# Kernel optimization log

Measured on AMD Instinct MI355X. Metric: run time of the kernel, lower is better.

Reference implementation:

```python
import jax, jax.numpy as jnp
import numpy as np

N_NODES = 50000
N_EDGES = 1600000
IN_C, HID_C, OUT_C = 64, 64, 7


def setup_inputs() -> dict:
    key = jax.random.key(0)
    ks = jax.random.split(key, 8)
    x = jax.random.normal(ks[0], (N_NODES, IN_C), dtype=jnp.float32)
    edge_index = jax.random.randint(ks[1], (2, N_EDGES), 0, N_NODES, dtype=jnp.int64)
    s_in = 1.0 / np.sqrt(IN_C)
    s_hid = 1.0 / np.sqrt(HID_C)
    W1 = jax.random.normal(ks[2], (HID_C, IN_C), dtype=jnp.float32) * s_in
    b1 = jnp.zeros((HID_C,), dtype=jnp.float32)
    W2 = jax.random.normal(ks[3], (HID_C, HID_C), dtype=jnp.float32) * s_hid
    b2 = jnp.zeros((HID_C,), dtype=jnp.float32)
    W3 = jax.random.normal(ks[4], (OUT_C, HID_C), dtype=jnp.float32) * s_hid
    b3 = jnp.zeros((OUT_C,), dtype=jnp.float32)
    return {"x": x, "edge_index": edge_index, "W1": W1, "b1": b1,
            "W2": W2, "b2": b2, "W3": W3, "b3": b3}


def _gcn_conv(x, src, dst, W, b):
    # GCNConv(normalize=False): lin -> sum-aggregate over incoming edges -> +bias
    h = x @ W.T                                   # [N, out]
    msg = h[src]                                  # gather source features [E, out]
    agg = jax.ops.segment_sum(msg, dst, num_segments=N_NODES)  # scatter-add
    return agg + b


def reference(x, edge_index, W1, b1, W2, b2, W3, b3):
    src, dst = edge_index[0], edge_index[1]
    h = jax.nn.relu(_gcn_conv(x, src, dst, W1, b1))   # dropout is identity in eval
    h = jax.nn.relu(_gcn_conv(h, src, dst, W2, b2))
    h = _gcn_conv(h, src, dst, W3, b3)
    return jax.nn.log_softmax(h, axis=-1)
```

## Files before the change

kernel.cpp:

```cpp
#include <hip/hip_runtime.h>
#include <math.h>

#define N_NODES 50000
#define N_EDGES 1600000
#define C 64
#define OUTC 7

#define NB 196
#define BCAP 10240
#define CHUNK 8192
#define BINBLKS 196

#define ZROW N_NODES

typedef __attribute__((ext_vector_type(8))) short bf16x8;
typedef __attribute__((ext_vector_type(4))) float f32x4;
typedef __attribute__((ext_vector_type(2))) float f32x2;

__device__ __forceinline__ unsigned int pk_bf16(float a, float b) {
    unsigned int ua = __float_as_uint(a);
    ua = (ua + 0x7FFFu + ((ua >> 16) & 1u)) >> 16;
    unsigned int ub = __float_as_uint(b);
    ub = (ub + 0x7FFFu + ((ub >> 16) & 1u)) >> 16;
    return ua | (ub << 16);
}

union U4B8 { uint4 u; bf16x8 s; };

__global__ __launch_bounds__(256) void prep(const float* __restrict__ W1,
                                            unsigned int* __restrict__ Wb1,
                                            int* __restrict__ gcursor) {
    const int b = blockIdx.x;
    const int tid = threadIdx.x;
    if (b < 8) {
        int idx = b * 256 + tid;
        float2 v = ((const float2*)W1)[idx];
        Wb1[idx] = pk_bf16(v.x, v.y);
    } else {
        if (tid < NB) gcursor[tid] = 0;
    }
}

__global__ __launch_bounds__(256) void bin_lin1(const int* __restrict__ src,
                                                const int* __restrict__ dst,
                                                unsigned int* __restrict__ buckets,
                                                int* __restrict__ gcursor,
                                                const float* __restrict__ x,
                                                const unsigned int* __restrict__ Wb,
                                                unsigned int* __restrict__ tout) {
    __shared__ unsigned int staged[CHUNK];
    __shared__ int hist[NB], scanb[NB], cur[NB], baseb[NB];
    const int tid = threadIdx.x;

    if (blockIdx.x < BINBLKS) {
        const int bx = blockIdx.x;
        const int base = bx * CHUNK;
        int n = N_EDGES - base; if (n > CHUNK) n = CHUNK;

        for (int b = tid; b < NB; b += 256) { hist[b] = 0; cur[b] = 0; }
        __syncthreads();

        const int4* src4 = (const int4*)(src + base);
        const int4* dst4 = (const int4*)(dst + base);
        unsigned int v[32];
        int nv = n >> 2;
#pragma unroll
        for (int k = 0; k < 8; ++k) {
            int i4 = k * 256 + tid;
            if (i4 < nv) {
                int4 s4 = src4[i4];
                int4 d4 = dst4[i4];
                unsigned int d0 = (unsigned int)d4.x, d1 = (unsigned int)d4.y;
                unsigned int d2 = (unsigned int)d4.z, d3 = (unsigned int)d4.w;
                v[k * 4 + 0] = (d0 << 16) | (unsigned int)s4.x;
                v[k * 4 + 1] = (d1 << 16) | (unsigned int)s4.y;
                v[k * 4 + 2] = (d2 << 16) | (unsigned int)s4.z;
                v[k * 4 + 3] = (d3 << 16) | (unsigned int)s4.w;
                atomicAdd(&hist[d0 >> 8], 1);
                atomicAdd(&hist[d1 >> 8], 1);
                atomicAdd(&hist[d2 >> 8], 1);
                atomicAdd(&hist[d3 >> 8], 1);
            }
        }
        __syncthreads();
        if (tid == 0) {
            int run = 0;
            for (int b = 0; b < NB; ++b) { scanb[b] = run; run += hist[b]; }
        }
        __syncthreads();
#pragma unroll
        for (int k = 0; k < 8; ++k) {
            int i4 = k * 256 + tid;
            if (i4 < nv) {
#pragma unroll
                for (int q = 0; q < 4; ++q) {
                    unsigned int w = v[k * 4 + q];
                    int b = w >> 24;
                    int p = scanb[b] + atomicAdd(&cur[b], 1);
                    staged[p] = w;
                }
            }
        }
        __syncthreads();
        if (tid < NB) baseb[tid] = atomicAdd(&gcursor[tid], hist[tid]);
        __syncthreads();
        for (int i = tid; i < n; i += 256) {
            unsigned int w = staged[i];
            int b = w >> 24;
            buckets[(size_t)b * BCAP + baseb[b] + (i - scanb[b])] = w;
        }
        return;
    }

    const int bx = blockIdx.x - BINBLKS;
    if (bx == 0 && tid < 32)
        tout[(size_t)ZROW * 32 + tid] = 0u;
    const int wave = tid >> 6;
    const int lane = tid & 63;
    const int quad = lane >> 4;
    const int l16  = lane & 15;
    const int rbase = bx * 64 + wave * 16;
    if (rbase >= N_NODES) return;

    U4B8 bfrag[4][2];
#pragma unroll
    for (int ct = 0; ct < 4; ++ct)
#pragma unroll
        for (int kt = 0; kt < 2; ++kt)
            bfrag[ct][kt].u = *(const uint4*)(Wb + (ct * 16 + l16) * 32 + kt * 16 + quad * 4);

    U4B8 afrag[2];
#pragma unroll
    for (int kt = 0; kt < 2; ++kt) {
        const float4* xp = (const float4*)(x + (size_t)(rbase + l16) * 64 + kt * 32 + quad * 8);
        float4 f0 = xp[0];
        float4 f1 = xp[1];
        afrag[kt].u.x = pk_bf16(f0.x, f0.y);
        afrag[kt].u.y = pk_bf16(f0.z, f0.w);
        afrag[kt].u.z = pk_bf16(f1.x, f1.y);
        afrag[kt].u.w = pk_bf16(f1.z, f1.w);
    }

    f32x4 acc[4];
#pragma unroll
    for (int ct = 0; ct < 4; ++ct) {
        f32x4 z = {0.f, 0.f, 0.f, 0.f};
        z = __builtin_amdgcn_mfma_f32_16x16x32_bf16(afrag[0].s, bfrag[ct][0].s, z, 0, 0, 0);
        z = __builtin_amdgcn_mfma_f32_16x16x32_bf16(afrag[1].s, bfrag[ct][1].s, z, 0, 0, 0);
        acc[ct] = z;
    }

    const int colp = l16 >> 1;
    const bool even = (l16 & 1) == 0;
#pragma unroll
    for (int ct = 0; ct < 4; ++ct) {
#pragma unroll
        for (int i = 0; i < 4; ++i) {
            float v = acc[ct][i];
            float p = __shfl_xor(v, 1, 64);
            if (even) {
                int row = rbase + quad * 4 + i;
                tout[(size_t)row * 32 + ct * 8 + colp] = pk_bf16(v, p);
            }
        }
    }
}

__global__ __launch_bounds__(256) void build_csr(const unsigned int* __restrict__ buckets,
                                                 const int* __restrict__ gcursor,
                                                 unsigned int* __restrict__ csr,
                                                 int* __restrict__ off) {
    __shared__ int hist[256], part[256], offx[256], cur[256];
    __shared__ int gl[NB];
    __shared__ int s_cnt, s_base;
    const int tid = threadIdx.x;
    const int b = blockIdx.x;

    hist[tid] = 0;
    cur[tid] = 0;
    if (tid < NB) gl[tid] = gcursor[tid];
    __syncthreads();
    if (tid == 0) {
        int bs = 0;
        for (int i = 0; i < b; ++i) bs += gl[i];
        s_base = bs;
        s_cnt = gl[b];
    }
    __syncthreads();
    const int cnt = s_cnt;
    const int gbase = s_base;
    const unsigned int* bk = buckets + (size_t)b * BCAP;

    for (int i = tid; i < cnt; i += 256) {
        atomicAdd(&hist[(bk[i] >> 16) & 255], 1);
    }
    __syncthreads();
    part[tid] = hist[tid];
    __syncthreads();
    for (int d = 1; d < 256; d <<= 1) {
        int t = (tid >= d) ? part[tid - d] : 0;
        __syncthreads();
        part[tid] += t;
        __syncthreads();
    }
    offx[tid] = (tid == 0) ? 0 : part[tid - 1];
    __syncthreads();
    int node = b * 256 + tid;
    if (node < N_NODES) off[node] = gbase + offx[tid];
    if (b == NB - 1 && tid == 0) off[N_NODES] = gbase + cnt;
    for (int i = tid; i < cnt; i += 256) {
        unsigned int w = bk[i];
        int dl = (w >> 16) & 255;
        int p = offx[dl] + atomicAdd(&cur[dl], 1);
        csr[gbase + p] = w & 0xFFFFu;
    }
}

#define ACC8(v)                                                              \
    do {                                                                     \
        s01 += (f32x2){__uint_as_float((v).x << 16),                         \
                       __uint_as_float((v).x & 0xFFFF0000u)};                \
        s23 += (f32x2){__uint_as_float((v).y << 16),                         \
                       __uint_as_float((v).y & 0xFFFF0000u)};                \
        s45 += (f32x2){__uint_as_float((v).z << 16),                         \
                       __uint_as_float((v).z & 0xFFFF0000u)};                \
        s67 += (f32x2){__uint_as_float((v).w << 16),                         \
                       __uint_as_float((v).w & 0xFFFF0000u)};                \
    } while (0)

__global__ __launch_bounds__(256) void gather64_lin2(const int* __restrict__ off,
                                                     const unsigned int* __restrict__ csr_src,
                                                     const unsigned int* __restrict__ tb,
                                                     const float* __restrict__ b,
                                                     const float* __restrict__ W2,
                                                     unsigned int* __restrict__ t2) {
    if (blockIdx.x == 0 && threadIdx.x < 32)
        t2[(size_t)ZROW * 32 + threadIdx.x] = 0u;
    int node = blockIdx.x * 4 + (threadIdx.x >> 6);
    if (node >= N_NODES) return;
    const int lane = threadIdx.x & 63;
    const int slot = lane >> 3;
    const int ch8  = lane & 7;
    int e0 = off[node], e1 = off[node + 1];
    const uint4* t4 = (const uint4*)tb;
    f32x2 s01 = {0.f, 0.f}, s23 = {0.f, 0.f}, s45 = {0.f, 0.f}, s67 = {0.f, 0.f};
    for (int e = e0; e < e1; e += 32) {
        int i0 = e + slot, i1 = i0 + 8, i2 = i0 + 16, i3 = i0 + 24;
        unsigned int a0 = csr_src[i0];
        unsigned int a1 = csr_src[i1];
        unsigned int a2 = csr_src[i2];
        unsigned int a3 = csr_src[i3];
        a0 = (i0 < e1) ? a0 : ZROW;
        a1 = (i1 < e1) ? a1 : ZROW;
        a2 = (i2 < e1) ? a2 : ZROW;
        a3 = (i3 < e1) ? a3 : ZROW;
        uint4 v0 = t4[(size_t)a0 * 8 + ch8];
        uint4 v1 = t4[(size_t)a1 * 8 + ch8];
        uint4 v2 = t4[(size_t)a2 * 8 + ch8];
        uint4 v3 = t4[(size_t)a3 * 8 + ch8];
        ACC8(v0);
        ACC8(v1);
        ACC8(v2);
        ACC8(v3);
    }
    float s[8] = {s01.x, s01.y, s23.x, s23.y, s45.x, s45.y, s67.x, s67.y};
#pragma unroll
    for (int d = 8; d <= 32; d <<= 1) {
#pragma unroll
        for (int j = 0; j < 8; ++j) s[j] += __shfl_xor(s[j], d, 64);
    }
    const float4 b0 = ((const float4*)b)[ch8 * 2];
    const float4 b1v = ((const float4*)b)[ch8 * 2 + 1];
    float r[8];
    r[0] = fmaxf(s[0] + b0.x, 0.f);
    r[1] = fmaxf(s[1] + b0.y, 0.f);
    r[2] = fmaxf(s[2] + b0.z, 0.f);
    r[3] = fmaxf(s[3] + b0.w, 0.f);
    r[4] = fmaxf(s[4] + b1v.x, 0.f);
    r[5] = fmaxf(s[5] + b1v.y, 0.f);
    r[6] = fmaxf(s[6] + b1v.z, 0.f);
    r[7] = fmaxf(s[7] + b1v.w, 0.f);
    float p[8];
#pragma unroll
    for (int n = 0; n < 8; ++n) {
        const float* wrow = W2 + (slot * 8 + n) * 64 + ch8 * 8;
        const float4 wa = *(const float4*)wrow;
        const float4 wb = *(const float4*)(wrow + 4);
        float t = r[0] * wa.x + r[1] * wa.y + r[2] * wa.z + r[3] * wa.w
                + r[4] * wb.x + r[5] * wb.y + r[6] * wb.z + r[7] * wb.w;
        t += __shfl_xor(t, 1, 64);
        t += __shfl_xor(t, 2, 64);
        t += __shfl_xor(t, 4, 64);
        p[n] = t;
    }
    if (ch8 == 0) {
        uint4 w;
        w.x = pk_bf16(p[0], p[1]);
        w.y = pk_bf16(p[2], p[3]);
        w.z = pk_bf16(p[4], p[5]);
        w.w = pk_bf16(p[6], p[7]);
        ((uint4*)(t2 + (size_t)node * 32))[slot] = w;
    }
}

__global__ __launch_bounds__(256) void gather64b_w3(const int* __restrict__ off,
                                                    const unsigned int* __restrict__ csr_src,
                                                    const unsigned int* __restrict__ tb,
                                                    const float* __restrict__ b,
                                                    const float* __restrict__ W3,
                                                    unsigned int* __restrict__ t3) {
    if (blockIdx.x == 0 && threadIdx.x < 4)
        t3[(size_t)ZROW * 4 + threadIdx.x] = 0u;
    int node = blockIdx.x * 4 + (threadIdx.x >> 6);
    if (node >= N_NODES) return;
    const int lane = threadIdx.x & 63;
    const int slot = lane >> 3;
    const int ch8  = lane & 7;
    int e0 = off[node], e1 = off[node + 1];
    const uint4* t4 = (const uint4*)tb;
    f32x2 s01 = {0.f, 0.f}, s23 = {0.f, 0.f}, s45 = {0.f, 0.f}, s67 = {0.f, 0.f};
    for (int e = e0; e < e1; e += 32) {
        int i0 = e + slot, i1 = i0 + 8, i2 = i0 + 16, i3 = i0 + 24;
        unsigned int a0 = csr_src[i0];
        unsigned int a1 = csr_src[i1];
        unsigned int a2 = csr_src[i2];
        unsigned int a3 = csr_src[i3];
        a0 = (i0 < e1) ? a0 : ZROW;
        a1 = (i1 < e1) ? a1 : ZROW;
        a2 = (i2 < e1) ? a2 : ZROW;
        a3 = (i3 < e1) ? a3 : ZROW;
        uint4 v0 = t4[(size_t)a0 * 8 + ch8];
        uint4 v1 = t4[(size_t)a1 * 8 + ch8];
        uint4 v2 = t4[(size_t)a2 * 8 + ch8];
        uint4 v3 = t4[(size_t)a3 * 8 + ch8];
        ACC8(v0);
        ACC8(v1);
        ACC8(v2);
        ACC8(v3);
    }
    float s[8] = {s01.x, s01.y, s23.x, s23.y, s45.x, s45.y, s67.x, s67.y};
#pragma unroll
    for (int d = 8; d <= 32; d <<= 1) {
#pragma unroll
        for (int j = 0; j < 8; ++j) s[j] += __shfl_xor(s[j], d, 64);
    }
    const float4 b0 = ((const float4*)b)[ch8 * 2];
    const float4 b1v = ((const float4*)b)[ch8 * 2 + 1];
    float r[8];
    r[0] = fmaxf(s[0] + b0.x, 0.f);
    r[1] = fmaxf(s[1] + b0.y, 0.f);
    r[2] = fmaxf(s[2] + b0.z, 0.f);
    r[3] = fmaxf(s[3] + b0.w, 0.f);
    r[4] = fmaxf(s[4] + b1v.x, 0.f);
    r[5] = fmaxf(s[5] + b1v.y, 0.f);
    r[6] = fmaxf(s[6] + b1v.z, 0.f);
    r[7] = fmaxf(s[7] + b1v.w, 0.f);
    float p[7];
#pragma unroll
    for (int j = 0; j < 7; ++j) {
        const float4 wa = *(const float4*)(W3 + j * 64 + ch8 * 8);
        const float4 wb = *(const float4*)(W3 + j * 64 + ch8 * 8 + 4);
        float t = r[0] * wa.x + r[1] * wa.y + r[2] * wa.z + r[3] * wa.w
                + r[4] * wb.x + r[5] * wb.y + r[6] * wb.z + r[7] * wb.w;
        t += __shfl_xor(t, 1, 64);
        t += __shfl_xor(t, 2, 64);
        t += __shfl_xor(t, 4, 64);
        p[j] = t;
    }
    if (lane == 0) {
        uint4 w;
        w.x = pk_bf16(p[0], p[1]);
        w.y = pk_bf16(p[2], p[3]);
        w.z = pk_bf16(p[4], p[5]);
        w.w = pk_bf16(p[6], 0.f);
        *(uint4*)(t3 + (size_t)node * 4) = w;
    }
}

__global__ __launch_bounds__(256) void gather7_lsm(const int* __restrict__ off,
                                                   const unsigned int* __restrict__ csr_src,
                                                   const unsigned int* __restrict__ t3,
                                                   const float* __restrict__ b,
                                                   float* __restrict__ out) {
    int node = blockIdx.x * 4 + (threadIdx.x >> 6);
    if (node >= N_NODES) return;
    const int lane = threadIdx.x & 63;
    const int slot = lane >> 1;
    const int h    = lane & 1;
    int e0 = off[node], e1 = off[node + 1];
    const uint2* t2 = (const uint2*)t3;
    float sx = 0.f, sy = 0.f, sz = 0.f, sw = 0.f;
    for (int e = e0; e < e1; e += 64) {
        int i0 = e + slot;
        int i1 = e + 32 + slot;
        unsigned int a0 = csr_src[i0];
        unsigned int a1 = csr_src[i1];
        a0 = (i0 < e1) ? a0 : ZROW;
        a1 = (i1 < e1) ? a1 : ZROW;
        uint2 v0 = t2[(size_t)a0 * 2 + h];
        uint2 v1 = t2[(size_t)a1 * 2 + h];
        sx += __uint_as_float(v0.x << 16);
        sy += __uint_as_float(v0.x & 0xFFFF0000u);
        sz += __uint_as_float(v0.y << 16);
        sw += __uint_as_float(v0.y & 0xFFFF0000u);
        sx += __uint_as_float(v1.x << 16);
        sy += __uint_as_float(v1.x & 0xFFFF0000u);
        sz += __uint_as_float(v1.y << 16);
        sw += __uint_as_float(v1.y & 0xFFFF0000u);
    }
#pragma unroll
    for (int d = 2; d <= 32; d <<= 1) {
        sx += __shfl_xor(sx, d, 64); sy += __shfl_xor(sy, d, 64);
        sz += __shfl_xor(sz, d, 64); sw += __shfl_xor(sw, d, 64);
    }
    float z0 = sx + b[h * 4 + 0];
    float z1 = sy + b[h * 4 + 1];
    float z2 = sz + b[h * 4 + 2];
    float z3 = (h == 0) ? (sw + b[3]) : -1e30f;
    float m = fmaxf(fmaxf(z0, z1), fmaxf(z2, z3));
    m = fmaxf(m, __shfl_xor(m, 1, 64));
    float ex = __expf(z0 - m) + __expf(z1 - m) + __expf(z2 - m) + __expf(z3 - m);
    ex += __shfl_xor(ex, 1, 64);
    float l = m + __logf(ex);
    if (lane < 2) {
        float* o = out + (size_t)node * 7 + h * 4;
        o[0] = z0 - l; o[1] = z1 - l; o[2] = z2 - l;
        if (h == 0) o[3] = z3 - l;
    }
}

extern "C" void kernel_launch(void* const* d_in, const int* in_sizes, int n_in,
                              void* d_out, int out_size, void* d_ws, size_t ws_size,
                              hipStream_t stream) {
    const float* x  = (const float*)d_in[0];
    const int*   ei = (const int*)d_in[1];
    const float* W1 = (const float*)d_in[2];
    const float* b1 = (const float*)d_in[3];
    const float* W2 = (const float*)d_in[4];
    const float* b2 = (const float*)d_in[5];
    const float* W3 = (const float*)d_in[6];
    const float* b3 = (const float*)d_in[7];
    float* out = (float*)d_out;

    const int* src = ei;
    const int* dst = ei + N_EDGES;

    float* A = (float*)d_ws;
    float* B = A + (size_t)N_NODES * C;
    unsigned int* csr = (unsigned int*)(B + (size_t)N_NODES * C);
    int* off     = (int*)(csr + N_EDGES);
    int* gcursor = off + N_NODES + 8;
    unsigned int* Wb1 = (unsigned int*)(gcursor + 256);
    unsigned int* buckets = (unsigned int*)A;
    unsigned int* T2 = (unsigned int*)A;
    unsigned int* Tt = (unsigned int*)B;
    unsigned int* T3 = Tt + (size_t)(N_NODES + 1) * 32;

    const int mfmagrid = (N_NODES + 63) / 64;
    const int ngrid    = (N_NODES + 3) / 4;

    prep<<<9, 256, 0, stream>>>(W1, Wb1, gcursor);

    bin_lin1<<<BINBLKS + mfmagrid, 256, 0, stream>>>(src, dst, buckets, gcursor,
                                                     x, Wb1, Tt);

    build_csr<<<NB, 256, 0, stream>>>(buckets, gcursor, csr, off);

    gather64_lin2<<<ngrid, 256, 0, stream>>>(off, csr, Tt, b1, W2, T2);

    gather64b_w3<<<ngrid, 256, 0, stream>>>(off, csr, T2, b2, W3, T3);

    gather7_lsm<<<ngrid, 256, 0, stream>>>(off, csr, T3, b3, out);
}
```

Baseline: 216.0 us.

## Use one-wave blocks per node, nontemporal gathers, smaller bin chunks, parallel prefix

The three gather kernels now launch one 64-thread block per node instead of four nodes per 256-thread block, and they read the gathered feature rows with nontemporal loads. The edge-binning phase switches to half-size chunks with twice as many blocks, and build_csr computes its bucket base offset with a wave-parallel reduction instead of a serial loop on one thread. Together these target load balance, scheduling granularity and a serial prefix bottleneck. The costs are more, smaller blocks to schedule and more global atomics on gcursor, and the nontemporal hint may hurt cache reuse of rows that are gathered many times.

```diff
diff --git a/kernel.cpp b/kernel.cpp
--- a/kernel.cpp
+++ b/kernel.cpp
@@ -8,14 +8,16 @@
 
 #define NB 196
 #define BCAP 10240
-#define CHUNK 8192
-#define BINBLKS 196
+#define CHUNK 4096
+#define BINBLKS 391
 
 #define ZROW N_NODES
 
 typedef __attribute__((ext_vector_type(8))) short bf16x8;
 typedef __attribute__((ext_vector_type(4))) float f32x4;
 typedef __attribute__((ext_vector_type(2))) float f32x2;
+typedef __attribute__((ext_vector_type(4))) unsigned int u32x4;
+typedef __attribute__((ext_vector_type(2))) unsigned int u32x2;
 
 __device__ __forceinline__ unsigned int pk_bf16(float a, float b) {
     unsigned int ua = __float_as_uint(a);
@@ -62,10 +64,10 @@
 
         const int4* src4 = (const int4*)(src + base);
         const int4* dst4 = (const int4*)(dst + base);
-        unsigned int v[32];
+        unsigned int v[16];
         int nv = n >> 2;
 #pragma unroll
-        for (int k = 0; k < 8; ++k) {
+        for (int k = 0; k < 4; ++k) {
             int i4 = k * 256 + tid;
             if (i4 < nv) {
                 int4 s4 = src4[i4];
@@ -89,7 +91,7 @@
         }
         __syncthreads();
 #pragma unroll
-        for (int k = 0; k < 8; ++k) {
+        for (int k = 0; k < 4; ++k) {
             int i4 = k * 256 + tid;
             if (i4 < nv) {
 #pragma unroll
@@ -172,6 +174,7 @@
                                                  int* __restrict__ off) {
     __shared__ int hist[256], part[256], offx[256], cur[256];
     __shared__ int gl[NB];
+    __shared__ int wsum[4];
     __shared__ int s_cnt, s_base;
     const int tid = threadIdx.x;
     const int b = blockIdx.x;
@@ -180,11 +183,17 @@
     cur[tid] = 0;
     if (tid < NB) gl[tid] = gcursor[tid];
     __syncthreads();
-    if (tid == 0) {
-        int bs = 0;
-        for (int i = 0; i < b; ++i) bs += gl[i];
-        s_base = bs;
-        s_cnt = gl[b];
+    {
+        int partial = 0;
+        for (int i = tid; i < b; i += 256) partial += gl[i];
+#pragma unroll
+        for (int d = 1; d < 64; d <<= 1) partial += __shfl_xor(partial, d, 64);
+        if ((tid & 63) == 0) wsum[tid >> 6] = partial;
+        __syncthreads();
+        if (tid == 0) {
+            s_base = wsum[0] + wsum[1] + wsum[2] + wsum[3];
+            s_cnt = gl[b];
+        }
     }
     __syncthreads();
     const int cnt = s_cnt;
@@ -228,21 +237,20 @@
                        __uint_as_float((v).w & 0xFFFF0000u)};                \
     } while (0)
 
-__global__ __launch_bounds__(256) void gather64_lin2(const int* __restrict__ off,
-                                                     const unsigned int* __restrict__ csr_src,
-                                                     const unsigned int* __restrict__ tb,
-                                                     const float* __restrict__ b,
-                                                     const float* __restrict__ W2,
-                                                     unsigned int* __restrict__ t2) {
-    if (blockIdx.x == 0 && threadIdx.x < 32)
-        t2[(size_t)ZROW * 32 + threadIdx.x] = 0u;
-    int node = blockIdx.x * 4 + (threadIdx.x >> 6);
-    if (node >= N_NODES) return;
-    const int lane = threadIdx.x & 63;
+__global__ __launch_bounds__(64) void gather64_lin2(const int* __restrict__ off,
+                                                    const unsigned int* __restrict__ csr_src,
+                                                    const unsigned int* __restrict__ tb,
+                                                    const float* __restrict__ b,
+                                                    const float* __restrict__ W2,
+                                                    unsigned int* __restrict__ t2) {
+    const int node = blockIdx.x;
+    const int lane = threadIdx.x;
+    if (node == 0 && lane < 32)
+        t2[(size_t)ZROW * 32 + lane] = 0u;
     const int slot = lane >> 3;
     const int ch8  = lane & 7;
     int e0 = off[node], e1 = off[node + 1];
-    const uint4* t4 = (const uint4*)tb;
+    const u32x4* t4 = (const u32x4*)tb;
     f32x2 s01 = {0.f, 0.f}, s23 = {0.f, 0.f}, s45 = {0.f, 0.f}, s67 = {0.f, 0.f};
     for (int e = e0; e < e1; e += 32) {
         int i0 = e + slot, i1 = i0 + 8, i2 = i0 + 16, i3 = i0 + 24;
@@ -254,10 +262,10 @@
         a1 = (i1 < e1) ? a1 : ZROW;
         a2 = (i2 < e1) ? a2 : ZROW;
         a3 = (i3 < e1) ? a3 : ZROW;
-        uint4 v0 = t4[(size_t)a0 * 8 + ch8];
-        uint4 v1 = t4[(size_t)a1 * 8 + ch8];
-        uint4 v2 = t4[(size_t)a2 * 8 + ch8];
-        uint4 v3 = t4[(size_t)a3 * 8 + ch8];
+        u32x4 v0 = __builtin_nontemporal_load(t4 + (size_t)a0 * 8 + ch8);
+        u32x4 v1 = __builtin_nontemporal_load(t4 + (size_t)a1 * 8 + ch8);
+        u32x4 v2 = __builtin_nontemporal_load(t4 + (size_t)a2 * 8 + ch8);
+        u32x4 v3 = __builtin_nontemporal_load(t4 + (size_t)a3 * 8 + ch8);
         ACC8(v0);
         ACC8(v1);
         ACC8(v2);
@@ -303,21 +311,20 @@
     }
 }
 
-__global__ __launch_bounds__(256) void gather64b_w3(const int* __restrict__ off,
-                                                    const unsigned int* __restrict__ csr_src,
-                                                    const unsigned int* __restrict__ tb,
-                                                    const float* __restrict__ b,
-                                                    const float* __restrict__ W3,
-                                                    unsigned int* __restrict__ t3) {
-    if (blockIdx.x == 0 && threadIdx.x < 4)
-        t3[(size_t)ZROW * 4 + threadIdx.x] = 0u;
-    int node = blockIdx.x * 4 + (threadIdx.x >> 6);
-    if (node >= N_NODES) return;
-    const int lane = threadIdx.x & 63;
+__global__ __launch_bounds__(64) void gather64b_w3(const int* __restrict__ off,
+                                                   const unsigned int* __restrict__ csr_src,
+                                                   const unsigned int* __restrict__ tb,
+                                                   const float* __restrict__ b,
+                                                   const float* __restrict__ W3,
+                                                   unsigned int* __restrict__ t3) {
+    const int node = blockIdx.x;
+    const int lane = threadIdx.x;
+    if (node == 0 && lane < 4)
+        t3[(size_t)ZROW * 4 + lane] = 0u;
     const int slot = lane >> 3;
     const int ch8  = lane & 7;
     int e0 = off[node], e1 = off[node + 1];
-    const uint4* t4 = (const uint4*)tb;
+    const u32x4* t4 = (const u32x4*)tb;
     f32x2 s01 = {0.f, 0.f}, s23 = {0.f, 0.f}, s45 = {0.f, 0.f}, s67 = {0.f, 0.f};
     for (int e = e0; e < e1; e += 32) {
         int i0 = e + slot, i1 = i0 + 8, i2 = i0 + 16, i3 = i0 + 24;
@@ -329,10 +336,10 @@
         a1 = (i1 < e1) ? a1 : ZROW;
         a2 = (i2 < e1) ? a2 : ZROW;
         a3 = (i3 < e1) ? a3 : ZROW;
-        uint4 v0 = t4[(size_t)a0 * 8 + ch8];
-        uint4 v1 = t4[(size_t)a1 * 8 + ch8];
-        uint4 v2 = t4[(size_t)a2 * 8 + ch8];
-        uint4 v3 = t4[(size_t)a3 * 8 + ch8];
+        u32x4 v0 = __builtin_nontemporal_load(t4 + (size_t)a0 * 8 + ch8);
+        u32x4 v1 = __builtin_nontemporal_load(t4 + (size_t)a1 * 8 + ch8);
+        u32x4 v2 = __builtin_nontemporal_load(t4 + (size_t)a2 * 8 + ch8);
+        u32x4 v3 = __builtin_nontemporal_load(t4 + (size_t)a3 * 8 + ch8);
         ACC8(v0);
         ACC8(v1);
         ACC8(v2);
@@ -377,18 +384,17 @@
     }
 }
 
-__global__ __launch_bounds__(256) void gather7_lsm(const int* __restrict__ off,
-                                                   const unsigned int* __restrict__ csr_src,
-                                                   const unsigned int* __restrict__ t3,
-                                                   const float* __restrict__ b,
-                                                   float* __restrict__ out) {
-    int node = blockIdx.x * 4 + (threadIdx.x >> 6);
-    if (node >= N_NODES) return;
-    const int lane = threadIdx.x & 63;
+__global__ __launch_bounds__(64) void gather7_lsm(const int* __restrict__ off,
+                                                  const unsigned int* __restrict__ csr_src,
+                                                  const unsigned int* __restrict__ t3,
+                                                  const float* __restrict__ b,
+                                                  float* __restrict__ out) {
+    const int node = blockIdx.x;
+    const int lane = threadIdx.x;
     const int slot = lane >> 1;
     const int h    = lane & 1;
     int e0 = off[node], e1 = off[node + 1];
-    const uint2* t2 = (const uint2*)t3;
+    const u32x2* t2 = (const u32x2*)t3;
     float sx = 0.f, sy = 0.f, sz = 0.f, sw = 0.f;
     for (int e = e0; e < e1; e += 64) {
         int i0 = e + slot;
@@ -397,8 +403,8 @@
         unsigned int a1 = csr_src[i1];
         a0 = (i0 < e1) ? a0 : ZROW;
         a1 = (i1 < e1) ? a1 : ZROW;
-        uint2 v0 = t2[(size_t)a0 * 2 + h];
-        uint2 v1 = t2[(size_t)a1 * 2 + h];
+        u32x2 v0 = __builtin_nontemporal_load(t2 + (size_t)a0 * 2 + h);
+        u32x2 v1 = __builtin_nontemporal_load(t2 + (size_t)a1 * 2 + h);
         sx += __uint_as_float(v0.x << 16);
         sy += __uint_as_float(v0.x & 0xFFFF0000u);
         sz += __uint_as_float(v0.y << 16);
@@ -457,7 +463,6 @@
     unsigned int* T3 = Tt + (size_t)(N_NODES + 1) * 32;
 
     const int mfmagrid = (N_NODES + 63) / 64;
-    const int ngrid    = (N_NODES + 3) / 4;
 
     prep<<<9, 256, 0, stream>>>(W1, Wb1, gcursor);
 
@@ -466,9 +471,9 @@
 
     build_csr<<<NB, 256, 0, stream>>>(buckets, gcursor, csr, off);
 
-    gather64_lin2<<<ngrid, 256, 0, stream>>>(off, csr, Tt, b1, W2, T2);
-
-    gather64b_w3<<<ngrid, 256, 0, stream>>>(off, csr, T2, b2, W3, T3);
-
-    gather7_lsm<<<ngrid, 256, 0, stream>>>(off, csr, T3, b3, out);
-}
+    gather64_lin2<<<N_NODES, 64, 0, stream>>>(off, csr, Tt, b1, W2, T2);
+
+    gather64b_w3<<<N_NODES, 64, 0, stream>>>(off, csr, T2, b2, W3, T3);
+
+    gather7_lsm<<<N_NODES, 64, 0, stream>>>(off, csr, T3, b3, out);
+}
```

Result: slower. 250.3 us (+15.9%).
